# Kernel tuning notes

Measured on AMD Instinct MI355X. Metric: run time of the kernel, lower is better.

The kernel has to match this reference:

```python
import jax, jax.numpy as jnp
import numpy as np

HEAD_DIM = 64
EMBED_DIM = 1024


def setup_inputs() -> dict:
    key = jax.random.key(0)
    k0, k1, k2, k3, k4, k5, k6 = jax.random.split(key, 7)
    B, T = 4, 2048
    s = 1.0 / np.sqrt(EMBED_DIM)
    return {
        "inputs": jax.random.normal(k0, (B, T, EMBED_DIM), dtype=jnp.float32),
        "Wq": jax.random.uniform(k1, (HEAD_DIM, EMBED_DIM), jnp.float32, -s, s),
        "bq": jax.random.uniform(k2, (HEAD_DIM,), jnp.float32, -s, s),
        "Wk": jax.random.uniform(k3, (HEAD_DIM, EMBED_DIM), jnp.float32, -s, s),
        "bk": jax.random.uniform(k4, (HEAD_DIM,), jnp.float32, -s, s),
        "Wv": jax.random.uniform(k5, (HEAD_DIM, EMBED_DIM), jnp.float32, -s, s),
        "bv": jax.random.uniform(k6, (HEAD_DIM,), jnp.float32, -s, s),
    }


def reference(inputs, Wq, bq, Wk, bk, Wv, bv):
    # inputs: [B, T, E]
    q = jnp.einsum("bte,he->bth", inputs, Wq) + bq  # [B, T, H]
    k = jnp.einsum("bte,he->bth", inputs, Wk) + bk
    v = jnp.einsum("bte,he->bth", inputs, Wv) + bv
    scores = jnp.einsum("bth,bsh->bts", q, k)  # [B, T, T]
    T = scores.shape[-1]
    causal = jnp.tril(jnp.ones((T, T), dtype=bool))  # True = keep
    scores = jnp.where(causal, scores, -jnp.inf)
    weights = jax.nn.softmax(scores / jnp.sqrt(jnp.float32(HEAD_DIM)), axis=-1)
    # dropout is identity in eval mode
    return jnp.einsum("bts,bsh->bth", weights, v)
```

## Files before the change

kernel.cpp:

```cpp
#include <hip/hip_runtime.h>
#include <hip/hip_bf16.h>

#define BATCH 4
#define SEQ   2048
#define EMB   1024
#define HD    64
#define BT    (BATCH * SEQ)
#define XS_STRIDE 1040

#define QSCALE 0.18033688011112042f

typedef __attribute__((ext_vector_type(8))) short bf16x8;
typedef __attribute__((ext_vector_type(4))) float f32x4;

__device__ __forceinline__ ushort f2bf(float f) {
    unsigned u = __float_as_uint(f);
    return (ushort)((u + 0x7FFFu + ((u >> 16) & 1u)) >> 16);
}

__global__ __launch_bounds__(256) void prep(
    const float* __restrict__ Wq, const float* __restrict__ bq,
    const float* __restrict__ Wk, const float* __restrict__ bk,
    const float* __restrict__ Wv, const float* __restrict__ bv,
    ushort* __restrict__ Wf, float* __restrict__ bb)
{
    const int fid = (int)blockIdx.x * 256 + (int)threadIdx.x;
    const int kc   = fid / 768;
    const int rem  = fid - kc * 768;
    const int sub  = rem >> 6;
    const int lane = rem & 63;
    const int row  = (sub & 3) * 16 + (lane & 15);
    const int e0   = kc * 32 + (lane >> 4) * 8;
    const float* W = (sub < 4) ? Wq : ((sub < 8) ? Wk : Wv);
    const float4 a0 = *(const float4*)(W + (size_t)row * EMB + e0);
    const float4 a1 = *(const float4*)(W + (size_t)row * EMB + e0 + 4);
    bf16x8 w;
    w[0] = (short)f2bf(a0.x); w[1] = (short)f2bf(a0.y);
    w[2] = (short)f2bf(a0.z); w[3] = (short)f2bf(a0.w);
    w[4] = (short)f2bf(a1.x); w[5] = (short)f2bf(a1.y);
    w[6] = (short)f2bf(a1.z); w[7] = (short)f2bf(a1.w);
    *(bf16x8*)(Wf + (size_t)fid * 8) = w;
    if (blockIdx.x == 0 && threadIdx.x < 192) {
        const int i = (int)threadIdx.x;
        const float* B = (i < 64) ? bq : ((i < 128) ? bk : bv);
        bb[i] = B[i & 63];
    }
}

__global__ __launch_bounds__(256) void qkv_gemm(
    const float* __restrict__ x, const ushort* __restrict__ Wf,
    const float* __restrict__ bb,
    ushort* __restrict__ Qf, ushort* __restrict__ Kf, ushort* __restrict__ Vf)
{
    const int t0   = (int)blockIdx.x * 16;
    const int tid  = (int)threadIdx.x;
    const int wv   = tid >> 6;
    const int lane = tid & 63;
    const int col  = lane & 15, quad = lane >> 4;

    __shared__ ushort xs[16][XS_STRIDE];

    #pragma unroll 4
    for (int it = 0; it < 16; ++it) {
        const int idx = it * 256 + tid;
        const int row = idx >> 8, c4 = idx & 255;
        const float4 v = *(const float4*)(x + (size_t)(t0 + row) * EMB + c4 * 4);
        ushort4 pk;
        pk.x = f2bf(v.x); pk.y = f2bf(v.y); pk.z = f2bf(v.z); pk.w = f2bf(v.w);
        *(ushort4*)&xs[row][c4 * 4] = pk;
    }
    __syncthreads();

    f32x4 acc[3];
    #pragma unroll
    for (int s = 0; s < 3; ++s) acc[s] = (f32x4){0.f, 0.f, 0.f, 0.f};
    const int sub0 = wv * 3;

    #pragma unroll 8
    for (int kc = 0; kc < 32; ++kc) {
        const bf16x8 a = *(const bf16x8*)&xs[col][kc * 32 + quad * 8];
        #pragma unroll
        for (int s = 0; s < 3; ++s) {
            const bf16x8 w = *(const bf16x8*)(Wf + ((size_t)(kc * 12 + sub0 + s) * 64 + lane) * 8);
            acc[s] = __builtin_amdgcn_mfma_f32_16x16x32_bf16(a, w, acc[s], 0, 0, 0);
        }
    }

    const int b  = t0 >> 11;
    const int qt = (t0 >> 4) & 127;
    const int sg = t0 + quad * 4;
    const int itk = (sg & (SEQ - 1)) >> 6;
    #pragma unroll
    for (int s = 0; s < 3; ++s) {
        const int sub  = sub0 + s;
        const int hrow = sub * 16 + col;
        const float bias = bb[hrow];
        if (sub < 4) {
            const int h = hrow;
            const int f = h >> 5, qd = (h >> 3) & 3, j = h & 7;
            ushort* base = Qf + (((size_t)(b * 128 + qt) * 2 + f) * 64 + qd * 16 + quad * 4) * 8 + j;
            #pragma unroll
            for (int i = 0; i < 4; ++i)
                base[i * 8] = f2bf((acc[s][i] + bias) * QSCALE);
        } else if (sub < 8) {
            const int h = hrow - 64;
            const int f = h >> 5, qd = (h >> 3) & 3, j = h & 7;
            const size_t frag = ((size_t)(b * 32 + itk) * 4 + ((sg >> 4) & 3)) * 2 + f;
            ushort* base = Kf + frag * 512 + ((size_t)((sg & 15) + 16 * qd)) * 8 + j;
            #pragma unroll
            for (int i = 0; i < 4; ++i)
                base[i * 8] = f2bf(acc[s][i] + bias);
        } else {
            const int h = hrow - 128;
            const int k0 = sg & 63;
            const int f = k0 >> 5, qd = (k0 >> 3) & 3, j0 = k0 & 7;
            const size_t frag = ((size_t)(b * 32 + itk) * 4 + (h >> 4)) * 2 + f;
            ushort4 pk;
            pk.x = f2bf(acc[s][0] + bias); pk.y = f2bf(acc[s][1] + bias);
            pk.z = f2bf(acc[s][2] + bias); pk.w = f2bf(acc[s][3] + bias);
            *(ushort4*)(Vf + frag * 512 + ((size_t)((h & 15) + 16 * qd)) * 8 + j0) = pk;
        }
    }
}

__global__ __launch_bounds__(256) void attn(
    const ushort* __restrict__ Qf, const ushort* __restrict__ Kf,
    const ushort* __restrict__ Vf, float* __restrict__ out)
{
    const int blk  = (int)blockIdx.x;
    const int b    = blk & 3;
    const int tile = 127 - (blk >> 2);
    const int t0   = tile * 16;
    const int nt   = (tile >> 2) + 1;
    const int tid  = (int)threadIdx.x;
    const int j    = tid >> 6;
    const int lane = tid & 63;
    const int col  = lane & 15, quad = lane >> 4;

    const ushort* Qb = Qf + ((size_t)(b * 128 + tile) * 2) * 512;
    const bf16x8 aq0 = *(const bf16x8*)(Qb + (size_t)lane * 8);
    const bf16x8 aq1 = *(const bf16x8*)(Qb + 512 + (size_t)lane * 8);

    float l_r[4];
    f32x4 o[4];
    #pragma unroll
    for (int i = 0; i < 4; ++i) { l_r[i] = 0.f; o[i] = (f32x4){0.f,0.f,0.f,0.f}; }

    __shared__ ushort pt[4][16][80];
    __shared__ __align__(16) float op[4][16][68];
    __shared__ float ll[4][16];

    bf16x8 kc[4][2];
    if (j < nt) {
        const ushort* Kt = Kf + ((size_t)(b * 32 + j) * 8) * 512;
        #pragma unroll
        for (int sub = 0; sub < 4; ++sub) {
            kc[sub][0] = *(const bf16x8*)(Kt + (size_t)(sub * 2 + 0) * 512 + (size_t)lane * 8);
            kc[sub][1] = *(const bf16x8*)(Kt + (size_t)(sub * 2 + 1) * 512 + (size_t)lane * 8);
        }
    }

    for (int it = j; it < nt; it += 4) {
        const int s0 = it * 64;
        const bool hasNext = (it + 4 < nt);

        f32x4 sc[4];
        #pragma unroll
        for (int sub = 0; sub < 4; ++sub) {
            f32x4 z = {0.f, 0.f, 0.f, 0.f};
            z = __builtin_amdgcn_mfma_f32_16x16x32_bf16(aq0, kc[sub][0], z, 0, 0, 0);
            z = __builtin_amdgcn_mfma_f32_16x16x32_bf16(aq1, kc[sub][1], z, 0, 0, 0);
            sc[sub] = z;
        }

        bf16x8 kn[4][2], vf[4][2];
        {
            const ushort* Vt = Vf + ((size_t)(b * 32 + it) * 8) * 512;
            #pragma unroll
            for (int sub = 0; sub < 4; ++sub) {
                vf[sub][0] = *(const bf16x8*)(Vt + (size_t)(sub * 2 + 0) * 512 + (size_t)lane * 8);
                vf[sub][1] = *(const bf16x8*)(Vt + (size_t)(sub * 2 + 1) * 512 + (size_t)lane * 8);
            }
        }
        if (hasNext) {
            const ushort* Kt = Kf + ((size_t)(b * 32 + it + 4) * 8) * 512;
            #pragma unroll
            for (int sub = 0; sub < 4; ++sub) {
                kn[sub][0] = *(const bf16x8*)(Kt + (size_t)(sub * 2 + 0) * 512 + (size_t)lane * 8);
                kn[sub][1] = *(const bf16x8*)(Kt + (size_t)(sub * 2 + 1) * 512 + (size_t)lane * 8);
            }
        }

        if (it == nt - 1) {
            #pragma unroll
            for (int sub = 0; sub < 4; ++sub)
                #pragma unroll
                for (int i = 0; i < 4; ++i) {
                    const int s = s0 + sub * 16 + col, t = t0 + quad * 4 + i;
                    if (s > t) sc[sub][i] = -1e30f;
                }
        }

        #pragma unroll
        for (int sub = 0; sub < 4; ++sub)
            #pragma unroll
            for (int i = 0; i < 4; ++i) {
                const float p = exp2f(sc[sub][i]);
                l_r[i] += p;
                pt[j][quad * 4 + i][sub * 16 + col] = f2bf(p);
            }

        __asm__ volatile("s_waitcnt lgkmcnt(0)" ::: "memory");
        const bf16x8 ap0 = *(const bf16x8*)&pt[j][col][quad * 8];
        const bf16x8 ap1 = *(const bf16x8*)&pt[j][col][32 + quad * 8];

        #pragma unroll
        for (int sub = 0; sub < 4; ++sub) {
            o[sub] = __builtin_amdgcn_mfma_f32_16x16x32_bf16(ap0, vf[sub][0], o[sub], 0, 0, 0);
            o[sub] = __builtin_amdgcn_mfma_f32_16x16x32_bf16(ap1, vf[sub][1], o[sub], 0, 0, 0);
        }

        if (hasNext) {
            #pragma unroll
            for (int sub = 0; sub < 4; ++sub) { kc[sub][0] = kn[sub][0]; kc[sub][1] = kn[sub][1]; }
        }
    }

    #pragma unroll
    for (int d = 1; d < 16; d <<= 1)
        #pragma unroll
        for (int i = 0; i < 4; ++i) l_r[i] += __shfl_xor(l_r[i], d, 64);

    #pragma unroll
    for (int sub = 0; sub < 4; ++sub)
        #pragma unroll
        for (int i = 0; i < 4; ++i)
            op[j][quad * 4 + i][sub * 16 + col] = o[sub][i];
    if (col == 0) {
        #pragma unroll
        for (int i = 0; i < 4; ++i)
            ll[j][quad * 4 + i] = l_r[i];
    }
    __syncthreads();

    {
        const int row = tid >> 4, c0 = (tid & 15) * 4;
        const float4 p0 = *(const float4*)&op[0][row][c0];
        const float4 p1 = *(const float4*)&op[1][row][c0];
        const float4 p2 = *(const float4*)&op[2][row][c0];
        const float4 p3 = *(const float4*)&op[3][row][c0];
        const float ls = ll[0][row] + ll[1][row] + ll[2][row] + ll[3][row];
        const float rinv = 1.0f / ls;
        float4 res;
        res.x = (p0.x + p1.x + p2.x + p3.x) * rinv;
        res.y = (p0.y + p1.y + p2.y + p3.y) * rinv;
        res.z = (p0.z + p1.z + p2.z + p3.z) * rinv;
        res.w = (p0.w + p1.w + p2.w + p3.w) * rinv;
        *(float4*)(out + ((size_t)b * SEQ + t0 + row) * HD + c0) = res;
    }
}

extern "C" void kernel_launch(void* const* d_in, const int* in_sizes, int n_in,
                              void* d_out, int out_size, void* d_ws, size_t ws_size,
                              hipStream_t stream)
{
    const float* x  = (const float*)d_in[0];
    const float* Wq = (const float*)d_in[1];
    const float* bq = (const float*)d_in[2];
    const float* Wk = (const float*)d_in[3];
    const float* bk = (const float*)d_in[4];
    const float* Wv = (const float*)d_in[5];
    const float* bv = (const float*)d_in[6];
    float* out = (float*)d_out;

    char* ws = (char*)d_ws;
    ushort* Wf  = (ushort*)(ws);
    float*  bb  = (float*)(ws + 0x60000);
    ushort* Qfb = (ushort*)(ws + 0x61000);
    ushort* Kfb = (ushort*)(ws + 0x161000);
    ushort* Vfb = (ushort*)(ws + 0x261000);

    prep<<<96, 256, 0, stream>>>(Wq, bq, Wk, bk, Wv, bv, Wf, bb);
    qkv_gemm<<<BT / 16, 256, 0, stream>>>(x, Wf, bb, Qfb, Kfb, Vfb);
    attn<<<512, 256, 0, stream>>>(Qfb, Kfb, Vfb, out);
}
```

Baseline: 108.1 us.

## Double row tiles per block in QKV GEMM and attention with 512-thread blocks

The QKV projection now processes 32 rows per block with 8 waves that split the K dimension in two halves. The second half of x is loaded while the first half is being multiplied, and the two partial sums are reduced through shared memory. The attention kernel processes two 16-row query tiles per block over 8 waves, so each K/V fragment load feeds twice the MFMA work. This trades more registers and shared memory per block, fewer blocks, and coarser causal-load balance for less redundant K/V and weight traffic.

```diff
diff --git a/kernel.cpp b/kernel.cpp
--- a/kernel.cpp
+++ b/kernel.cpp
@@ -47,108 +47,178 @@
     }
 }
 
-__global__ __launch_bounds__(256) void qkv_gemm(
+__global__ __launch_bounds__(512, 2) void qkv_gemm(
     const float* __restrict__ x, const ushort* __restrict__ Wf,
     const float* __restrict__ bb,
     ushort* __restrict__ Qf, ushort* __restrict__ Kf, ushort* __restrict__ Vf)
 {
-    const int t0   = (int)blockIdx.x * 16;
+    const int t0   = (int)blockIdx.x * 32;
     const int tid  = (int)threadIdx.x;
     const int wv   = tid >> 6;
     const int lane = tid & 63;
     const int col  = lane & 15, quad = lane >> 4;
-
-    __shared__ ushort xs[16][XS_STRIDE];
+    const int sg   = wv >> 1;
+    const int kp   = wv & 1;
+    const int sub0 = sg * 3;
+
+    __shared__ ushort xs[32][XS_STRIDE];
+    __shared__ __align__(16) float red[4][64][24];
+
+    float4 v0[8];
+    #pragma unroll
+    for (int i = 0; i < 8; ++i) {
+        const int idx = i * 512 + tid;
+        const int row = idx >> 7, c4 = idx & 127;
+        v0[i] = *(const float4*)(x + (size_t)(t0 + row) * EMB + c4 * 4);
+    }
+    #pragma unroll
+    for (int i = 0; i < 8; ++i) {
+        const int idx = i * 512 + tid;
+        const int row = idx >> 7, c4 = idx & 127;
+        ushort4 pk;
+        pk.x = f2bf(v0[i].x); pk.y = f2bf(v0[i].y);
+        pk.z = f2bf(v0[i].z); pk.w = f2bf(v0[i].w);
+        *(ushort4*)&xs[row][c4 * 4] = pk;
+    }
+    __syncthreads();
+
+    float4 v1[8];
+    #pragma unroll
+    for (int i = 0; i < 8; ++i) {
+        const int idx = i * 512 + tid;
+        const int row = idx >> 7, c4 = idx & 127;
+        v1[i] = *(const float4*)(x + (size_t)(t0 + row) * EMB + 512 + c4 * 4);
+    }
+
+    f32x4 acc[2][3];
+    #pragma unroll
+    for (int rg = 0; rg < 2; ++rg)
+        #pragma unroll
+        for (int s = 0; s < 3; ++s) acc[rg][s] = (f32x4){0.f, 0.f, 0.f, 0.f};
 
     #pragma unroll 4
-    for (int it = 0; it < 16; ++it) {
-        const int idx = it * 256 + tid;
-        const int row = idx >> 8, c4 = idx & 255;
-        const float4 v = *(const float4*)(x + (size_t)(t0 + row) * EMB + c4 * 4);
-        ushort4 pk;
-        pk.x = f2bf(v.x); pk.y = f2bf(v.y); pk.z = f2bf(v.z); pk.w = f2bf(v.w);
-        *(ushort4*)&xs[row][c4 * 4] = pk;
-    }
-    __syncthreads();
-
-    f32x4 acc[3];
-    #pragma unroll
-    for (int s = 0; s < 3; ++s) acc[s] = (f32x4){0.f, 0.f, 0.f, 0.f};
-    const int sub0 = wv * 3;
-
-    #pragma unroll 8
-    for (int kc = 0; kc < 32; ++kc) {
-        const bf16x8 a = *(const bf16x8*)&xs[col][kc * 32 + quad * 8];
+    for (int t = 0; t < 8; ++t) {
+        const int kc = kp + 2 * t;
+        const bf16x8 a0 = *(const bf16x8*)&xs[col][kc * 32 + quad * 8];
+        const bf16x8 a1 = *(const bf16x8*)&xs[16 + col][kc * 32 + quad * 8];
         #pragma unroll
         for (int s = 0; s < 3; ++s) {
             const bf16x8 w = *(const bf16x8*)(Wf + ((size_t)(kc * 12 + sub0 + s) * 64 + lane) * 8);
-            acc[s] = __builtin_amdgcn_mfma_f32_16x16x32_bf16(a, w, acc[s], 0, 0, 0);
-        }
-    }
-
-    const int b  = t0 >> 11;
-    const int qt = (t0 >> 4) & 127;
-    const int sg = t0 + quad * 4;
-    const int itk = (sg & (SEQ - 1)) >> 6;
-    #pragma unroll
-    for (int s = 0; s < 3; ++s) {
-        const int sub  = sub0 + s;
-        const int hrow = sub * 16 + col;
-        const float bias = bb[hrow];
-        if (sub < 4) {
-            const int h = hrow;
-            const int f = h >> 5, qd = (h >> 3) & 3, j = h & 7;
-            ushort* base = Qf + (((size_t)(b * 128 + qt) * 2 + f) * 64 + qd * 16 + quad * 4) * 8 + j;
-            #pragma unroll
-            for (int i = 0; i < 4; ++i)
-                base[i * 8] = f2bf((acc[s][i] + bias) * QSCALE);
-        } else if (sub < 8) {
-            const int h = hrow - 64;
-            const int f = h >> 5, qd = (h >> 3) & 3, j = h & 7;
-            const size_t frag = ((size_t)(b * 32 + itk) * 4 + ((sg >> 4) & 3)) * 2 + f;
-            ushort* base = Kf + frag * 512 + ((size_t)((sg & 15) + 16 * qd)) * 8 + j;
-            #pragma unroll
-            for (int i = 0; i < 4; ++i)
-                base[i * 8] = f2bf(acc[s][i] + bias);
-        } else {
-            const int h = hrow - 128;
-            const int k0 = sg & 63;
-            const int f = k0 >> 5, qd = (k0 >> 3) & 3, j0 = k0 & 7;
-            const size_t frag = ((size_t)(b * 32 + itk) * 4 + (h >> 4)) * 2 + f;
-            ushort4 pk;
-            pk.x = f2bf(acc[s][0] + bias); pk.y = f2bf(acc[s][1] + bias);
-            pk.z = f2bf(acc[s][2] + bias); pk.w = f2bf(acc[s][3] + bias);
-            *(ushort4*)(Vf + frag * 512 + ((size_t)((h & 15) + 16 * qd)) * 8 + j0) = pk;
-        }
-    }
-}
-
-__global__ __launch_bounds__(256) void attn(
+            acc[0][s] = __builtin_amdgcn_mfma_f32_16x16x32_bf16(a0, w, acc[0][s], 0, 0, 0);
+            acc[1][s] = __builtin_amdgcn_mfma_f32_16x16x32_bf16(a1, w, acc[1][s], 0, 0, 0);
+        }
+    }
+
+    #pragma unroll
+    for (int i = 0; i < 8; ++i) {
+        const int idx = i * 512 + tid;
+        const int row = idx >> 7, c4 = idx & 127;
+        ushort4 pk;
+        pk.x = f2bf(v1[i].x); pk.y = f2bf(v1[i].y);
+        pk.z = f2bf(v1[i].z); pk.w = f2bf(v1[i].w);
+        *(ushort4*)&xs[row][512 + c4 * 4] = pk;
+    }
+    __syncthreads();
+
+    #pragma unroll 4
+    for (int t = 0; t < 8; ++t) {
+        const int kc = 16 + kp + 2 * t;
+        const bf16x8 a0 = *(const bf16x8*)&xs[col][kc * 32 + quad * 8];
+        const bf16x8 a1 = *(const bf16x8*)&xs[16 + col][kc * 32 + quad * 8];
+        #pragma unroll
+        for (int s = 0; s < 3; ++s) {
+            const bf16x8 w = *(const bf16x8*)(Wf + ((size_t)(kc * 12 + sub0 + s) * 64 + lane) * 8);
+            acc[0][s] = __builtin_amdgcn_mfma_f32_16x16x32_bf16(a0, w, acc[0][s], 0, 0, 0);
+            acc[1][s] = __builtin_amdgcn_mfma_f32_16x16x32_bf16(a1, w, acc[1][s], 0, 0, 0);
+        }
+    }
+
+    if (kp) {
+        #pragma unroll
+        for (int rg = 0; rg < 2; ++rg)
+            #pragma unroll
+            for (int s = 0; s < 3; ++s)
+                *(f32x4*)&red[sg][lane][(rg * 3 + s) * 4] = acc[rg][s];
+    }
+    __syncthreads();
+    if (kp) return;
+    #pragma unroll
+    for (int rg = 0; rg < 2; ++rg)
+        #pragma unroll
+        for (int s = 0; s < 3; ++s)
+            acc[rg][s] += *(const f32x4*)&red[sg][lane][(rg * 3 + s) * 4];
+
+    #pragma unroll
+    for (int rg = 0; rg < 2; ++rg) {
+        const int tt0 = t0 + rg * 16;
+        const int b   = tt0 >> 11;
+        const int qt  = (tt0 >> 4) & 127;
+        const int sgt = tt0 + quad * 4;
+        const int itk = (sgt & (SEQ - 1)) >> 6;
+        #pragma unroll
+        for (int s = 0; s < 3; ++s) {
+            const int sub  = sub0 + s;
+            const int hrow = sub * 16 + col;
+            const float bias = bb[hrow];
+            if (sub < 4) {
+                const int h = hrow;
+                const int f = h >> 5, qd = (h >> 3) & 3, jj = h & 7;
+                ushort* base = Qf + (((size_t)(b * 128 + qt) * 2 + f) * 64 + qd * 16 + quad * 4) * 8 + jj;
+                #pragma unroll
+                for (int i = 0; i < 4; ++i)
+                    base[i * 8] = f2bf((acc[rg][s][i] + bias) * QSCALE);
+            } else if (sub < 8) {
+                const int h = hrow - 64;
+                const int f = h >> 5, qd = (h >> 3) & 3, jj = h & 7;
+                const size_t frag = ((size_t)(b * 32 + itk) * 4 + ((sgt >> 4) & 3)) * 2 + f;
+                ushort* base = Kf + frag * 512 + ((size_t)((sgt & 15) + 16 * qd)) * 8 + jj;
+                #pragma unroll
+                for (int i = 0; i < 4; ++i)
+                    base[i * 8] = f2bf(acc[rg][s][i] + bias);
+            } else {
+                const int h = hrow - 128;
+                const int k0 = sgt & 63;
+                const int f = k0 >> 5, qd = (k0 >> 3) & 3, j0 = k0 & 7;
+                const size_t frag = ((size_t)(b * 32 + itk) * 4 + (h >> 4)) * 2 + f;
+                ushort4 pk;
+                pk.x = f2bf(acc[rg][s][0] + bias); pk.y = f2bf(acc[rg][s][1] + bias);
+                pk.z = f2bf(acc[rg][s][2] + bias); pk.w = f2bf(acc[rg][s][3] + bias);
+                *(ushort4*)(Vf + frag * 512 + ((size_t)((h & 15) + 16 * qd)) * 8 + j0) = pk;
+            }
+        }
+    }
+}
+
+__global__ __launch_bounds__(512, 2) void attn(
     const ushort* __restrict__ Qf, const ushort* __restrict__ Kf,
     const ushort* __restrict__ Vf, float* __restrict__ out)
 {
     const int blk  = (int)blockIdx.x;
     const int b    = blk & 3;
-    const int tile = 127 - (blk >> 2);
-    const int t0   = tile * 16;
-    const int nt   = (tile >> 2) + 1;
+    const int tl   = 63 - (blk >> 2);
+    const int t0   = tl * 32;
+    const int nt   = ((t0 + 31) >> 6) + 1;
     const int tid  = (int)threadIdx.x;
     const int j    = tid >> 6;
     const int lane = tid & 63;
     const int col  = lane & 15, quad = lane >> 4;
 
-    const ushort* Qb = Qf + ((size_t)(b * 128 + tile) * 2) * 512;
-    const bf16x8 aq0 = *(const bf16x8*)(Qb + (size_t)lane * 8);
-    const bf16x8 aq1 = *(const bf16x8*)(Qb + 512 + (size_t)lane * 8);
-
-    float l_r[4];
-    f32x4 o[4];
-    #pragma unroll
-    for (int i = 0; i < 4; ++i) { l_r[i] = 0.f; o[i] = (f32x4){0.f,0.f,0.f,0.f}; }
-
-    __shared__ ushort pt[4][16][80];
-    __shared__ __align__(16) float op[4][16][68];
-    __shared__ float ll[4][16];
+    const ushort* QbA = Qf + ((size_t)(b * 128 + 2 * tl) * 2) * 512;
+    const bf16x8 aqA0 = *(const bf16x8*)(QbA + (size_t)lane * 8);
+    const bf16x8 aqA1 = *(const bf16x8*)(QbA + 512 + (size_t)lane * 8);
+    const bf16x8 aqB0 = *(const bf16x8*)(QbA + 1024 + (size_t)lane * 8);
+    const bf16x8 aqB1 = *(const bf16x8*)(QbA + 1536 + (size_t)lane * 8);
+
+    float l_a[4], l_b[4];
+    f32x4 o[8];
+    #pragma unroll
+    for (int i = 0; i < 4; ++i) { l_a[i] = 0.f; l_b[i] = 0.f; }
+    #pragma unroll
+    for (int i = 0; i < 8; ++i) o[i] = (f32x4){0.f, 0.f, 0.f, 0.f};
+
+    __shared__ ushort pt[8][32][80];
+    __shared__ __align__(16) float op[8][32][68];
+    __shared__ float ll[8][32];
 
     bf16x8 kc[4][2];
     if (j < nt) {
@@ -160,17 +230,21 @@
         }
     }
 
-    for (int it = j; it < nt; it += 4) {
+    for (int it = j; it < nt; it += 8) {
         const int s0 = it * 64;
-        const bool hasNext = (it + 4 < nt);
-
-        f32x4 sc[4];
+        const bool hasNext = (it + 8 < nt);
+
+        f32x4 scA[4], scB[4];
         #pragma unroll
         for (int sub = 0; sub < 4; ++sub) {
             f32x4 z = {0.f, 0.f, 0.f, 0.f};
-            z = __builtin_amdgcn_mfma_f32_16x16x32_bf16(aq0, kc[sub][0], z, 0, 0, 0);
-            z = __builtin_amdgcn_mfma_f32_16x16x32_bf16(aq1, kc[sub][1], z, 0, 0, 0);
-            sc[sub] = z;
+            z = __builtin_amdgcn_mfma_f32_16x16x32_bf16(aqA0, kc[sub][0], z, 0, 0, 0);
+            z = __builtin_amdgcn_mfma_f32_16x16x32_bf16(aqA1, kc[sub][1], z, 0, 0, 0);
+            scA[sub] = z;
+            f32x4 y = {0.f, 0.f, 0.f, 0.f};
+            y = __builtin_amdgcn_mfma_f32_16x16x32_bf16(aqB0, kc[sub][0], y, 0, 0, 0);
+            y = __builtin_amdgcn_mfma_f32_16x16x32_bf16(aqB1, kc[sub][1], y, 0, 0, 0);
+            scB[sub] = y;
         }
 
         bf16x8 kn[4][2], vf[4][2];
@@ -183,7 +257,7 @@
             }
         }
         if (hasNext) {
-            const ushort* Kt = Kf + ((size_t)(b * 32 + it + 4) * 8) * 512;
+            const ushort* Kt = Kf + ((size_t)(b * 32 + it + 8) * 8) * 512;
             #pragma unroll
             for (int sub = 0; sub < 4; ++sub) {
                 kn[sub][0] = *(const bf16x8*)(Kt + (size_t)(sub * 2 + 0) * 512 + (size_t)lane * 8);
@@ -196,8 +270,10 @@
             for (int sub = 0; sub < 4; ++sub)
                 #pragma unroll
                 for (int i = 0; i < 4; ++i) {
-                    const int s = s0 + sub * 16 + col, t = t0 + quad * 4 + i;
-                    if (s > t) sc[sub][i] = -1e30f;
+                    const int s  = s0 + sub * 16 + col;
+                    const int tA = t0 + quad * 4 + i;
+                    if (s > tA)      scA[sub][i] = -1e30f;
+                    if (s > tA + 16) scB[sub][i] = -1e30f;
                 }
         }
 
@@ -205,19 +281,26 @@
         for (int sub = 0; sub < 4; ++sub)
             #pragma unroll
             for (int i = 0; i < 4; ++i) {
-                const float p = exp2f(sc[sub][i]);
-                l_r[i] += p;
-                pt[j][quad * 4 + i][sub * 16 + col] = f2bf(p);
+                const float pA = exp2f(scA[sub][i]);
+                l_a[i] += pA;
+                pt[j][quad * 4 + i][sub * 16 + col] = f2bf(pA);
+                const float pB = exp2f(scB[sub][i]);
+                l_b[i] += pB;
+                pt[j][16 + quad * 4 + i][sub * 16 + col] = f2bf(pB);
             }
 
         __asm__ volatile("s_waitcnt lgkmcnt(0)" ::: "memory");
-        const bf16x8 ap0 = *(const bf16x8*)&pt[j][col][quad * 8];
-        const bf16x8 ap1 = *(const bf16x8*)&pt[j][col][32 + quad * 8];
+        const bf16x8 apA0 = *(const bf16x8*)&pt[j][col][quad * 8];
+        const bf16x8 apA1 = *(const bf16x8*)&pt[j][col][32 + quad * 8];
+        const bf16x8 apB0 = *(const bf16x8*)&pt[j][16 + col][quad * 8];
+        const bf16x8 apB1 = *(const bf16x8*)&pt[j][16 + col][32 + quad * 8];
 
         #pragma unroll
         for (int sub = 0; sub < 4; ++sub) {
-            o[sub] = __builtin_amdgcn_mfma_f32_16x16x32_bf16(ap0, vf[sub][0], o[sub], 0, 0, 0);
-            o[sub] = __builtin_amdgcn_mfma_f32_16x16x32_bf16(ap1, vf[sub][1], o[sub], 0, 0, 0);
+            o[sub]     = __builtin_amdgcn_mfma_f32_16x16x32_bf16(apA0, vf[sub][0], o[sub], 0, 0, 0);
+            o[sub]     = __builtin_amdgcn_mfma_f32_16x16x32_bf16(apA1, vf[sub][1], o[sub], 0, 0, 0);
+            o[4 + sub] = __builtin_amdgcn_mfma_f32_16x16x32_bf16(apB0, vf[sub][0], o[4 + sub], 0, 0, 0);
+            o[4 + sub] = __builtin_amdgcn_mfma_f32_16x16x32_bf16(apB1, vf[sub][1], o[4 + sub], 0, 0, 0);
         }
 
         if (hasNext) {
@@ -229,33 +312,39 @@
     #pragma unroll
     for (int d = 1; d < 16; d <<= 1)
         #pragma unroll
-        for (int i = 0; i < 4; ++i) l_r[i] += __shfl_xor(l_r[i], d, 64);
+        for (int i = 0; i < 4; ++i) {
+            l_a[i] += __shfl_xor(l_a[i], d, 64);
+            l_b[i] += __shfl_xor(l_b[i], d, 64);
+        }
 
     #pragma unroll
     for (int sub = 0; sub < 4; ++sub)
         #pragma unroll
-        for (int i = 0; i < 4; ++i)
-            op[j][quad * 4 + i][sub * 16 + col] = o[sub][i];
+        for (int i = 0; i < 4; ++i) {
+            op[j][quad * 4 + i][sub * 16 + col]      = o[sub][i];
+            op[j][16 + quad * 4 + i][sub * 16 + col] = o[4 + sub][i];
+        }
     if (col == 0) {
         #pragma unroll
-        for (int i = 0; i < 4; ++i)
-            ll[j][quad * 4 + i] = l_r[i];
+        for (int i = 0; i < 4; ++i) {
+            ll[j][quad * 4 + i]      = l_a[i];
+            ll[j][16 + quad * 4 + i] = l_b[i];
+        }
     }
     __syncthreads();
 
     {
         const int row = tid >> 4, c0 = (tid & 15) * 4;
-        const float4 p0 = *(const float4*)&op[0][row][c0];
-        const float4 p1 = *(const float4*)&op[1][row][c0];
-        const float4 p2 = *(const float4*)&op[2][row][c0];
-        const float4 p3 = *(const float4*)&op[3][row][c0];
-        const float ls = ll[0][row] + ll[1][row] + ll[2][row] + ll[3][row];
+        float sx = 0.f, sy = 0.f, sz = 0.f, sw = 0.f, ls = 0.f;
+        #pragma unroll
+        for (int w = 0; w < 8; ++w) {
+            const float4 p = *(const float4*)&op[w][row][c0];
+            sx += p.x; sy += p.y; sz += p.z; sw += p.w;
+            ls += ll[w][row];
+        }
         const float rinv = 1.0f / ls;
         float4 res;
-        res.x = (p0.x + p1.x + p2.x + p3.x) * rinv;
-        res.y = (p0.y + p1.y + p2.y + p3.y) * rinv;
-        res.z = (p0.z + p1.z + p2.z + p3.z) * rinv;
-        res.w = (p0.w + p1.w + p2.w + p3.w) * rinv;
+        res.x = sx * rinv; res.y = sy * rinv; res.z = sz * rinv; res.w = sw * rinv;
         *(float4*)(out + ((size_t)b * SEQ + t0 + row) * HD + c0) = res;
     }
 }
@@ -281,6 +370,6 @@
     ushort* Vfb = (ushort*)(ws + 0x261000);
 
     prep<<<96, 256, 0, stream>>>(Wq, bq, Wk, bk, Wv, bv, Wf, bb);
-    qkv_gemm<<<BT / 16, 256, 0, stream>>>(x, Wf, bb, Qfb, Kfb, Vfb);
-    attn<<<512, 256, 0, stream>>>(Qfb, Kfb, Vfb, out);
-}
+    qkv_gemm<<<BT / 32, 512, 0, stream>>>(x, Wf, bb, Qfb, Kfb, Vfb);
+    attn<<<256, 512, 0, stream>>>(Qfb, Kfb, Vfb, out);
+}
```

After: 105.1 us. 2.7% less time.
